# Kernel tuning notes

Hardware: AMD Instinct MI355X
Metric: run time of the kernel (lower is better)

The kernel has to match this reference:

```python
import jax, jax.numpy as jnp
import numpy as np

B, T, C, H = 4, 1024, 1024, 16
D = C // H
EPS = 1e-5


def _ln(x, g, b):
    mu = jnp.mean(x, axis=-1, keepdims=True)
    var = jnp.mean((x - mu) ** 2, axis=-1, keepdims=True)
    return (x - mu) * jax.lax.rsqrt(var + EPS) * g + b


def _attn(xq, xkv, wq, wk, wv, wo, bo, mask):
    # wq/wk/wv/wo: [C, C] (in, out). Dropout is identity in eval mode.
    Bq, Tq, _ = xq.shape
    Tk = xkv.shape[1]
    q = (xq @ wq).reshape(Bq, Tq, H, D)
    k = (xkv @ wk).reshape(Bq, Tk, H, D)
    v = (xkv @ wv).reshape(Bq, Tk, H, D)
    scores = jnp.einsum('bqhd,bkhd->bhqk', q, k) / jnp.sqrt(jnp.float32(D))
    if mask is not None:
        scores = jnp.where(mask == 0, -jnp.inf, scores)
    p = jax.nn.softmax(scores, axis=-1)
    out = jnp.einsum('bhqk,bkhd->bqhd', p, v).reshape(Bq, Tq, C)
    return out @ wo + bo


def setup_inputs() -> dict:
    key = jax.random.key(0)
    ks = jax.random.split(key, 20)
    s = 0.02
    inp = {
        'x': jax.random.normal(ks[0], (B, T, C), jnp.float32),
        'encoder_out': jax.random.normal(ks[1], (B, T, C), jnp.float32),
        'sa_wq': jax.random.normal(ks[2], (C, C), jnp.float32) * s,
        'sa_wk': jax.random.normal(ks[3], (C, C), jnp.float32) * s,
        'sa_wv': jax.random.normal(ks[4], (C, C), jnp.float32) * s,
        'sa_wo': jax.random.normal(ks[5], (C, C), jnp.float32) * s,
        'sa_bo': jnp.zeros((C,), jnp.float32),
        'ca_wq': jax.random.normal(ks[6], (C, C), jnp.float32) * s,
        'ca_wk': jax.random.normal(ks[7], (C, C), jnp.float32) * s,
        'ca_wv': jax.random.normal(ks[8], (C, C), jnp.float32) * s,
        'ca_wo': jax.random.normal(ks[9], (C, C), jnp.float32) * s,
        'ca_bo': jnp.zeros((C,), jnp.float32),
        'ff_w1': jax.random.normal(ks[10], (C, 4 * C), jnp.float32) * s,
        'ff_b1': jnp.zeros((4 * C,), jnp.float32),
        'ff_w2': jax.random.normal(ks[11], (4 * C, C), jnp.float32) * s,
        'ff_b2': jnp.zeros((C,), jnp.float32),
        'ln1_g': jnp.ones((C,), jnp.float32), 'ln1_b': jnp.zeros((C,), jnp.float32),
        'ln2_g': jnp.ones((C,), jnp.float32), 'ln2_b': jnp.zeros((C,), jnp.float32),
        'ln3_g': jnp.ones((C,), jnp.float32), 'ln3_b': jnp.zeros((C,), jnp.float32),
        'tgt_mask': jnp.tril(jnp.ones((T, T), jnp.int32))[None, None],  # [1,1,T,T] causal
        'src_mask': jnp.ones((B, 1, 1, T), jnp.int32),
    }
    return inp


def reference(x, encoder_out, sa_wq, sa_wk, sa_wv, sa_wo, sa_bo,
              ca_wq, ca_wk, ca_wv, ca_wo, ca_bo,
              ff_w1, ff_b1, ff_w2, ff_b2,
              ln1_g, ln1_b, ln2_g, ln2_b, ln3_g, ln3_b,
              tgt_mask, src_mask):
    # self-attention (masked) + residual
    x = x + _attn(_ln(x, ln1_g, ln1_b), _ln(x, ln1_g, ln1_b),
                  sa_wq, sa_wk, sa_wv, sa_wo, sa_bo, tgt_mask)
    # cross-attention + residual (only src_mask applied to scores)
    h = _ln(x, ln2_g, ln2_b)
    x = x + _attn(h, encoder_out, ca_wq, ca_wk, ca_wv, ca_wo, ca_bo, src_mask)
    # FFN + residual
    h = _ln(x, ln3_g, ln3_b)
    x = x + (jax.nn.relu(h @ ff_w1 + ff_b1) @ ff_w2 + ff_b2)
    return x
```

## Files before the change

kernel.cpp:

```cpp
#include <hip/hip_runtime.h>

typedef __bf16 bf16_t;
typedef __bf16 bf16x4 __attribute__((ext_vector_type(4)));
typedef __bf16 bf16x8 __attribute__((ext_vector_type(8)));
typedef float  f32x4  __attribute__((ext_vector_type(4)));

#define LN_EPS 1e-5f

__device__ __forceinline__ void g2l16(const bf16_t* g, bf16_t* l) {
    __builtin_amdgcn_global_load_lds(
        (const __attribute__((address_space(1))) void*)g,
        (__attribute__((address_space(3))) void*)l, 16, 0, 0);
}

__global__ __launch_bounds__(256) void cvt_kernel(
    const float* __restrict__ x, bf16_t* __restrict__ y)
{
    int i = blockIdx.x * 256 + threadIdx.x;
    f32x4 v = ((const f32x4*)x)[i];
    bf16x4 o = { (bf16_t)v.x, (bf16_t)v.y, (bf16_t)v.z, (bf16_t)v.w };
    ((bf16x4*)y)[i] = o;
}

struct WT16 {
    const float* src[16]; bf16_t* dst[16];
    int srcN[16]; int dstK[16]; int k0b[16]; int n0b[16];
};

__global__ __launch_bounds__(256) void wt16_kernel(WT16 p)
{
    const int z = blockIdx.z;
    const float* W = p.src[z];
    bf16_t* Wt = p.dst[z];
    const int N = p.srcN[z], Kd = p.dstK[z];
    const int n0 = p.n0b[z] + blockIdx.x * 64, k0 = p.k0b[z] + blockIdx.y * 64;
    __shared__ float ts[64][65];
    const int tid = threadIdx.x;
#pragma unroll
    for (int it = 0; it < 4; ++it) {
        int f = tid + it * 256;
        int row = f >> 4, c4 = (f & 15) * 4;
        f32x4 v = *(const f32x4*)(W + (size_t)(k0 + row) * N + n0 + c4);
        ts[row][c4 + 0] = v.x; ts[row][c4 + 1] = v.y;
        ts[row][c4 + 2] = v.z; ts[row][c4 + 3] = v.w;
    }
    __syncthreads();
#pragma unroll
    for (int it = 0; it < 4; ++it) {
        int f = tid + it * 256;
        int nrow = f >> 4, k4 = (f & 15) * 4;
        bf16x4 o = { (bf16_t)ts[k4 + 0][nrow], (bf16_t)ts[k4 + 1][nrow],
                     (bf16_t)ts[k4 + 2][nrow], (bf16_t)ts[k4 + 3][nrow] };
        *(bf16x4*)(Wt + (size_t)(n0 + nrow) * Kd + k0 + k4) = o;
    }
}

__global__ __launch_bounds__(256) void ln_kernel(
    const float* __restrict__ x, const float* __restrict__ g,
    const float* __restrict__ b, bf16_t* __restrict__ y)
{
    const int row = blockIdx.x;
    const int tid = threadIdx.x;
    const f32x4* xr = (const f32x4*)(x + (size_t)row * 1024);
    f32x4 v = xr[tid];
    float s  = v.x + v.y + v.z + v.w;
    float s2 = v.x*v.x + v.y*v.y + v.z*v.z + v.w*v.w;
#pragma unroll
    for (int off = 1; off < 64; off <<= 1) {
        s  += __shfl_xor(s,  off, 64);
        s2 += __shfl_xor(s2, off, 64);
    }
    __shared__ float ws_[4], ws2_[4];
    const int wave = tid >> 6, lane = tid & 63;
    if (lane == 0) { ws_[wave] = s; ws2_[wave] = s2; }
    __syncthreads();
    s  = ws_[0] + ws_[1] + ws_[2] + ws_[3];
    s2 = ws2_[0] + ws2_[1] + ws2_[2] + ws2_[3];
    const float mu   = s  * (1.0f/1024.0f);
    const float var  = s2 * (1.0f/1024.0f) - mu*mu;
    const float rstd = rsqrtf(var + LN_EPS);
    f32x4 gv = ((const f32x4*)g)[tid];
    f32x4 bv = ((const f32x4*)b)[tid];
    f32x4 o  = (v - mu) * rstd * gv + bv;
    bf16x4 ob = { (bf16_t)o.x, (bf16_t)o.y, (bf16_t)o.z, (bf16_t)o.w };
    ((bf16x4*)(y + (size_t)row * 1024))[tid] = ob;
}

template<int BN, int DEPTH, int OUT_BF16, int HAS_BIAS, int DO_RELU, int HAS_RES>
__global__ __launch_bounds__(256) void gemm_bf16(
    const bf16_t* __restrict__ A, const bf16_t* __restrict__ Bt,
    const float* __restrict__ bias, const float* __restrict__ res,
    void* __restrict__ out, int M, int N, int K)
{
    constexpr int NT = BN / 32;
    __shared__ __align__(16) bf16_t As[2][DEPTH][128 * 32];
    __shared__ __align__(16) bf16_t Bs[2][DEPTH][BN * 32];

    const int tid  = threadIdx.x;
    const int wave = tid >> 6, lane = tid & 63;
    const int q    = lane >> 4, r = lane & 15;
    const int wm   = wave >> 1, wn = wave & 1;

    const int nbx  = gridDim.x;
    const int id   = blockIdx.y * nbx + blockIdx.x;
    const int mper = gridDim.y >> 3;
    const int jj   = id >> 3;
    const int bm   = (id & 7) * mper + jj / nbx;
    const int bn   = jj % nbx;
    const int m0   = bm * 128, n0 = bn * BN;

    const int srow = lane >> 2;
    const int schk = (lane & 3) * 8;

    auto stage = [&](int buf, int kk) {
#pragma unroll
        for (int s = 0; s < DEPTH; ++s) {
#pragma unroll
            for (int t = 0; t < 2; ++t) {
                int rowA = wave * 32 + t * 16;
                g2l16(A + (size_t)(m0 + rowA + srow) * K + kk + s * 32 + schk,
                      &As[buf][s][rowA * 32]);
            }
#pragma unroll
            for (int t = 0; t < BN / 64; ++t) {
                int rowB = wave * (BN / 4) + t * 16;
                g2l16(Bt + (size_t)(n0 + rowB + srow) * K + kk + s * 32 + schk,
                      &Bs[buf][s][rowB * 32]);
            }
        }
    };

    f32x4 acc[4][NT] = {};
    constexpr int STEP = 32 * DEPTH;
    stage(0, 0);

    for (int kk = 0; kk < K; kk += STEP) {
        const int cur = (kk / STEP) & 1;
        __syncthreads();
        if (kk + STEP < K) stage(cur ^ 1, kk + STEP);
#pragma unroll
        for (int s = 0; s < DEPTH; ++s) {
            bf16x8 af[4], bf[NT];
#pragma unroll
            for (int i = 0; i < 4; ++i)
                af[i] = *(const bf16x8*)&As[cur][s][(wm * 64 + i * 16 + r) * 32 + q * 8];
#pragma unroll
            for (int j = 0; j < NT; ++j)
                bf[j] = *(const bf16x8*)&Bs[cur][s][(wn * 16 * NT + j * 16 + r) * 32 + q * 8];
#pragma unroll
            for (int i = 0; i < 4; ++i)
#pragma unroll
                for (int j = 0; j < NT; ++j)
                    acc[i][j] = __builtin_amdgcn_mfma_f32_16x16x32_bf16(af[i], bf[j], acc[i][j], 0, 0, 0);
        }
    }

#pragma unroll
    for (int i = 0; i < 4; ++i)
#pragma unroll
        for (int j = 0; j < NT; ++j)
#pragma unroll
            for (int e = 0; e < 4; ++e) {
                int row = m0 + wm * 64 + i * 16 + q * 4 + e;
                int col = n0 + wn * 16 * NT + j * 16 + r;
                float v = acc[i][j][e];
                if (HAS_BIAS) v += bias[col];
                if (DO_RELU)  v = v > 0.0f ? v : 0.0f;
                if (HAS_RES)  v += res[(size_t)row * N + col];
                if (OUT_BF16) ((bf16_t*)out)[(size_t)row * N + col] = (bf16_t)v;
                else          ((float*)out)[(size_t)row * N + col] = v;
            }
}

__global__ __launch_bounds__(256) void gemm_qkv3(
    const bf16_t* __restrict__ Aq, const bf16_t* __restrict__ Akv,
    const bf16_t* __restrict__ Wt3,
    bf16_t* __restrict__ outq, bf16_t* __restrict__ outk,
    bf16_t* __restrict__ vt)
{
    const int K = 1024;
    __shared__ __align__(16) bf16_t As[2][128 * 32];
    __shared__ __align__(16) bf16_t Bs[2][128 * 32];

    const int tid  = threadIdx.x;
    const int wave = tid >> 6, lane = tid & 63;
    const int q    = lane >> 4, r = lane & 15;
    const int wm   = wave >> 1, wn = wave & 1;

    const int nbx  = gridDim.x;
    const int id   = blockIdx.y * nbx + blockIdx.x;
    const int mper = gridDim.y >> 3;
    const int jj   = id >> 3;
    const int bm   = (id & 7) * mper + jj / nbx;
    const int bn   = jj % nbx;
    const int m0   = bm * 128, n0 = bn * 128;
    const int grp  = bn >> 3;
    const bf16_t* A = (grp == 0) ? Aq : Akv;

    const int srow = lane >> 2;
    const int schk = (lane & 3) * 8;

    auto stage = [&](int buf, int kk) {
#pragma unroll
        for (int t = 0; t < 2; ++t) {
            int row = wave * 32 + t * 16;
            g2l16(A   + (size_t)(m0 + row + srow) * K + kk + schk, &As[buf][row * 32]);
            g2l16(Wt3 + (size_t)(n0 + row + srow) * K + kk + schk, &Bs[buf][row * 32]);
        }
    };

    f32x4 acc[4][4] = {};
    stage(0, 0);

    for (int kk = 0; kk < K; kk += 32) {
        const int cur = (kk >> 5) & 1;
        __syncthreads();
        if (kk + 32 < K) stage(cur ^ 1, kk + 32);

        bf16x8 af[4], bf[4];
#pragma unroll
        for (int i = 0; i < 4; ++i)
            af[i] = *(const bf16x8*)&As[cur][(wm * 64 + i * 16 + r) * 32 + q * 8];
#pragma unroll
        for (int j = 0; j < 4; ++j)
            bf[j] = *(const bf16x8*)&Bs[cur][(wn * 64 + j * 16 + r) * 32 + q * 8];
#pragma unroll
        for (int i = 0; i < 4; ++i)
#pragma unroll
            for (int j = 0; j < 4; ++j)
                acc[i][j] = __builtin_amdgcn_mfma_f32_16x16x32_bf16(af[i], bf[j], acc[i][j], 0, 0, 0);
    }

    if (grp < 2) {
        bf16_t* o = (grp == 0) ? outq : outk;
        const float sc = (grp == 0) ? 0.125f : 1.0f;
        const int c0 = n0 - grp * 1024;
#pragma unroll
        for (int i = 0; i < 4; ++i)
#pragma unroll
            for (int j = 0; j < 4; ++j)
#pragma unroll
                for (int e = 0; e < 4; ++e) {
                    int row = m0 + wm * 64 + i * 16 + q * 4 + e;
                    int col = c0 + wn * 64 + j * 16 + r;
                    o[(size_t)row * 1024 + col] = (bf16_t)(acc[i][j][e] * sc);
                }
    } else {
#pragma unroll
        for (int i = 0; i < 4; ++i)
#pragma unroll
            for (int j = 0; j < 4; ++j) {
                int c = (n0 - 2048) + wn * 64 + j * 16 + r;
                int hh = c >> 6, d = c & 63;
                int row0 = m0 + wm * 64 + i * 16 + q * 4;
                int bb = row0 >> 10, t = row0 & 1023;
                bf16x4 pk = { (bf16_t)acc[i][j][0], (bf16_t)acc[i][j][1],
                              (bf16_t)acc[i][j][2], (bf16_t)acc[i][j][3] };
                *(bf16x4*)&vt[((size_t)((bb << 4) + hh) * 64 + d) * 1024 + t] = pk;
            }
    }
}

template<int CAUSAL>
__global__ __launch_bounds__(256) void attn_mfma_kernel(
    const bf16_t* __restrict__ Qp, const bf16_t* __restrict__ Kp,
    const bf16_t* __restrict__ VTp, bf16_t* __restrict__ Op)
{
    const int T = 1024;
    const int LP = 72;
    __shared__ __align__(16) bf16_t Ps[128 * LP];
    __shared__ __align__(16) bf16_t Ks[2][2][64 * 32];
    __shared__ __align__(16) bf16_t Vs[2][2][64 * 32];

    const int id  = blockIdx.x + 8 * (blockIdx.y + 16 * blockIdx.z);
    const int jj  = id >> 3;
    const int pr  = (id & 7) * 8 + (jj >> 3);
    const int qt  = jj & 7;
    const int h   = pr & 15, b = pr >> 4;

    const int tid  = threadIdx.x;
    const int wave = tid >> 6, lane = tid & 63;
    const int q    = lane >> 4, r = lane & 15;
    const int srow = lane >> 2, schk = (lane & 3) * 8;

    const bf16_t* Kb = Kp + (size_t)(b * T) * 1024 + h * 64;
    const bf16_t* Vb = VTp + (size_t)((b * 16 + h) * 64) * 1024;

    auto stageKV = [&](int buf, int kt) {
#pragma unroll
        for (int ks = 0; ks < 2; ++ks) {
            g2l16(Kb + (size_t)(kt * 64 + wave * 16 + srow) * 1024 + ks * 32 + schk,
                  &Ks[buf][ks][wave * 16 * 32]);
            g2l16(Vb + (size_t)(wave * 16 + srow) * 1024 + kt * 64 + ks * 32 + schk,
                  &Vs[buf][ks][wave * 16 * 32]);
        }
    };

    {
        const bf16_t* Qb = Qp + (size_t)(b * T + qt * 128) * 1024 + h * 64;
#pragma unroll
        for (int it = 0; it < 4; ++it) {
            int f = tid + it * 256;
            int row = f >> 3, c8 = (f & 7) * 8;
            *(bf16x8*)&Ps[row * LP + c8] = *(const bf16x8*)(Qb + (size_t)row * 1024 + c8);
        }
    }
    __syncthreads();
    bf16x8 qa[2][2];
#pragma unroll
    for (int mt = 0; mt < 2; ++mt)
#pragma unroll
        for (int ks = 0; ks < 2; ++ks)
            qa[mt][ks] = *(const bf16x8*)&Ps[(wave * 32 + mt * 16 + r) * LP + ks * 32 + q * 8];

    const bf16_t one_b = (bf16_t)1.0f;
    const bf16x8 ones = { one_b, one_b, one_b, one_b, one_b, one_b, one_b, one_b };

    f32x4 o[2][4] = {};
    f32x4 ol[2] = {};

    const int nk = CAUSAL ? (2 * qt + 2) : 16;
    stageKV(0, 0);

    for (int kt = 0; kt < nk; ++kt) {
        const int cur = kt & 1;
        __syncthreads();
        if (kt + 1 < nk) stageKV(cur ^ 1, kt + 1);

        f32x4 s[2][4] = {};
#pragma unroll
        for (int ks = 0; ks < 2; ++ks)
#pragma unroll
            for (int nt = 0; nt < 4; ++nt) {
                bf16x8 kb = *(const bf16x8*)&Ks[cur][ks][(nt * 16 + r) * 32 + q * 8];
#pragma unroll
                for (int mt = 0; mt < 2; ++mt)
                    s[mt][nt] = __builtin_amdgcn_mfma_f32_16x16x32_bf16(qa[mt][ks], kb, s[mt][nt], 0, 0, 0);
            }

        if (CAUSAL) {
#pragma unroll
            for (int mt = 0; mt < 2; ++mt) {
                const int r0 = qt * 128 + wave * 32 + mt * 16;
                if (kt * 64 + 63 > r0) {
#pragma unroll
                    for (int nt = 0; nt < 4; ++nt) {
                        int kg = kt * 64 + nt * 16 + r;
#pragma unroll
                        for (int i2 = 0; i2 < 4; ++i2)
                            if (kg > r0 + q * 4 + i2) s[mt][nt][i2] = -INFINITY;
                    }
                }
            }
        }

#pragma unroll
        for (int mt = 0; mt < 2; ++mt)
#pragma unroll
            for (int nt = 0; nt < 4; ++nt)
#pragma unroll
                for (int i2 = 0; i2 < 4; ++i2)
                    Ps[(wave * 32 + mt * 16 + q * 4 + i2) * LP + nt * 16 + r] =
                        (bf16_t)__expf(s[mt][nt][i2]);

#pragma unroll
        for (int ks = 0; ks < 2; ++ks) {
            bf16x8 pa[2];
#pragma unroll
            for (int mt = 0; mt < 2; ++mt)
                pa[mt] = *(const bf16x8*)&Ps[(wave * 32 + mt * 16 + r) * LP + ks * 32 + q * 8];
#pragma unroll
            for (int dt = 0; dt < 4; ++dt) {
                bf16x8 vb = *(const bf16x8*)&Vs[cur][ks][(dt * 16 + r) * 32 + q * 8];
#pragma unroll
                for (int mt = 0; mt < 2; ++mt)
                    o[mt][dt] = __builtin_amdgcn_mfma_f32_16x16x32_bf16(pa[mt], vb, o[mt][dt], 0, 0, 0);
            }
#pragma unroll
            for (int mt = 0; mt < 2; ++mt)
                ol[mt] = __builtin_amdgcn_mfma_f32_16x16x32_bf16(pa[mt], ones, ol[mt], 0, 0, 0);
        }
    }

    bf16_t* Ob = Op + (size_t)(b * T + qt * 128 + wave * 32) * 1024 + h * 64;
#pragma unroll
    for (int mt = 0; mt < 2; ++mt) {
        f32x4 inv;
#pragma unroll
        for (int i2 = 0; i2 < 4; ++i2) inv[i2] = 1.0f / ol[mt][i2];
#pragma unroll
        for (int dt = 0; dt < 4; ++dt)
#pragma unroll
            for (int i2 = 0; i2 < 4; ++i2)
                Ob[(size_t)(mt * 16 + q * 4 + i2) * 1024 + dt * 16 + r] = (bf16_t)(o[mt][dt][i2] * inv[i2]);
    }
}

extern "C" void kernel_launch(void* const* d_in, const int* in_sizes, int n_in,
                              void* d_out, int out_size, void* d_ws, size_t ws_size,
                              hipStream_t stream)
{
    const float* x     = (const float*)d_in[0];
    const float* enc   = (const float*)d_in[1];
    const float* sa_wq = (const float*)d_in[2];
    const float* sa_wk = (const float*)d_in[3];
    const float* sa_wv = (const float*)d_in[4];
    const float* sa_wo = (const float*)d_in[5];
    const float* sa_bo = (const float*)d_in[6];
    const float* ca_wq = (const float*)d_in[7];
    const float* ca_wk = (const float*)d_in[8];
    const float* ca_wv = (const float*)d_in[9];
    const float* ca_wo = (const float*)d_in[10];
    const float* ca_bo = (const float*)d_in[11];
    const float* ff_w1 = (const float*)d_in[12];
    const float* ff_b1 = (const float*)d_in[13];
    const float* ff_w2 = (const float*)d_in[14];
    const float* ff_b2 = (const float*)d_in[15];
    const float* ln1_g = (const float*)d_in[16];
    const float* ln1_b = (const float*)d_in[17];
    const float* ln2_g = (const float*)d_in[18];
    const float* ln2_b = (const float*)d_in[19];
    const float* ln3_g = (const float*)d_in[20];
    const float* ln3_b = (const float*)d_in[21];

    float* out = (float*)d_out;
    char* ws = (char*)d_ws;
    const size_t MB = 1024 * 1024;
    bf16_t* w_s3  = (bf16_t*)(ws +  0 * MB);
    bf16_t* w_so  = (bf16_t*)(ws +  6 * MB);
    bf16_t* w_c3  = (bf16_t*)(ws +  8 * MB);
    bf16_t* w_co  = (bf16_t*)(ws + 14 * MB);
    bf16_t* w_f1  = (bf16_t*)(ws + 16 * MB);
    bf16_t* w_f2  = (bf16_t*)(ws + 24 * MB);
    bf16_t* b_enc = (bf16_t*)(ws + 32 * MB);
    bf16_t* b_ln  = (bf16_t*)(ws + 40 * MB);
    bf16_t* b_q   = (bf16_t*)(ws + 48 * MB);
    bf16_t* b_k   = (bf16_t*)(ws + 56 * MB);
    bf16_t* b_vt  = (bf16_t*)(ws + 64 * MB);
    bf16_t* b_at  = (bf16_t*)(ws + 72 * MB);
    float*  b_x1  = (float*) (ws + 80 * MB);
    float*  b_x2  = (float*) (ws + 48 * MB);
    bf16_t* b_h1  = (bf16_t*)(ws + 64 * MB);

    const int M = 4096;
    dim3 blk(256);

    WT16 wp;
    const float* srcs[8] = { sa_wq, sa_wk, sa_wv, sa_wo, ca_wq, ca_wk, ca_wv, ca_wo };
    bf16_t* dsts[8] = { w_s3, w_s3 + 1024*1024, w_s3 + 2048*1024, w_so,
                        w_c3, w_c3 + 1024*1024, w_c3 + 2048*1024, w_co };
    for (int z = 0; z < 8; ++z) {
        wp.src[z] = srcs[z]; wp.dst[z] = dsts[z];
        wp.srcN[z] = 1024; wp.dstK[z] = 1024; wp.k0b[z] = 0; wp.n0b[z] = 0;
    }
    for (int z = 8; z < 12; ++z) {
        wp.src[z] = ff_w1; wp.dst[z] = w_f1;
        wp.srcN[z] = 4096; wp.dstK[z] = 1024; wp.k0b[z] = 0; wp.n0b[z] = (z - 8) * 1024;
    }
    for (int z = 12; z < 16; ++z) {
        wp.src[z] = ff_w2; wp.dst[z] = w_f2;
        wp.srcN[z] = 1024; wp.dstK[z] = 4096; wp.k0b[z] = (z - 12) * 1024; wp.n0b[z] = 0;
    }
    wt16_kernel<<<dim3(16, 16, 16), blk, 0, stream>>>(wp);
    cvt_kernel<<<4096, blk, 0, stream>>>(enc, b_enc);

    ln_kernel<<<4096, blk, 0, stream>>>(x, ln1_g, ln1_b, b_ln);
    gemm_qkv3<<<dim3(24, 32), blk, 0, stream>>>(b_ln, b_ln, w_s3, b_q, b_k, b_vt);
    attn_mfma_kernel<1><<<dim3(8, 16, 4), blk, 0, stream>>>(b_q, b_k, b_vt, b_at);
    gemm_bf16<64,2,0,1,0,1><<<dim3(16, 32), blk, 0, stream>>>(
        b_at, w_so, sa_bo, x, b_x1, M, 1024, 1024);
    ln_kernel<<<4096, blk, 0, stream>>>(b_x1, ln2_g, ln2_b, b_ln);
    gemm_qkv3<<<dim3(24, 32), blk, 0, stream>>>(b_ln, b_enc, w_c3, b_q, b_k, b_vt);
    attn_mfma_kernel<0><<<dim3(8, 16, 4), blk, 0, stream>>>(b_q, b_k, b_vt, b_at);
    gemm_bf16<64,2,0,1,0,1><<<dim3(16, 32), blk, 0, stream>>>(
        b_at, w_co, ca_bo, b_x1, b_x2, M, 1024, 1024);
    ln_kernel<<<4096, blk, 0, stream>>>(b_x2, ln3_g, ln3_b, b_ln);
    gemm_bf16<128,1,1,1,1,0><<<dim3(32, 32), blk, 0, stream>>>(
        b_ln, w_f1, ff_b1, nullptr, b_h1, M, 4096, 1024);
    gemm_bf16<64,2,0,1,0,1><<<dim3(16, 32), blk, 0, stream>>>(
        b_h1, w_f2, ff_b2, b_x2, out, M, 1024, 4096);
}
```

Before: 482.9 us.

## Deepen GEMM LDS pipelines with vmcnt waits, swizzled LDS, and MFMA priority

```diff
diff --git a/kernel.cpp b/kernel.cpp
--- a/kernel.cpp
+++ b/kernel.cpp
@@ -11,6 +11,19 @@
     __builtin_amdgcn_global_load_lds(
         (const __attribute__((address_space(1))) void*)g,
         (__attribute__((address_space(3))) void*)l, 16, 0, 0);
+}
+
+template<int N> __device__ __forceinline__ void wait_vm() {
+    if constexpr (N == 0)      asm volatile("s_waitcnt vmcnt(0)" ::: "memory");
+    else if constexpr (N == 3) asm volatile("s_waitcnt vmcnt(3)" ::: "memory");
+    else if constexpr (N == 4) asm volatile("s_waitcnt vmcnt(4)" ::: "memory");
+    else if constexpr (N == 6) asm volatile("s_waitcnt vmcnt(6)" ::: "memory");
+    else if constexpr (N == 8) asm volatile("s_waitcnt vmcnt(8)" ::: "memory");
+    else                       asm volatile("s_waitcnt vmcnt(0)" ::: "memory");
+}
+__device__ __forceinline__ void block_bar() {
+    __builtin_amdgcn_s_barrier();
+    asm volatile("" ::: "memory");
 }
 
 __global__ __launch_bounds__(256) void cvt_kernel(
@@ -86,15 +99,16 @@
     ((bf16x4*)(y + (size_t)row * 1024))[tid] = ob;
 }
 
-template<int BN, int DEPTH, int OUT_BF16, int HAS_BIAS, int DO_RELU, int HAS_RES>
+template<int BN, int NBUF, int OUT_BF16, int HAS_BIAS, int DO_RELU, int HAS_RES>
 __global__ __launch_bounds__(256) void gemm_bf16(
     const bf16_t* __restrict__ A, const bf16_t* __restrict__ Bt,
     const float* __restrict__ bias, const float* __restrict__ res,
     void* __restrict__ out, int M, int N, int K)
 {
     constexpr int NT = BN / 32;
-    __shared__ __align__(16) bf16_t As[2][DEPTH][128 * 32];
-    __shared__ __align__(16) bf16_t Bs[2][DEPTH][BN * 32];
+    constexpr int L  = 2 + BN / 64;
+    __shared__ __align__(16) bf16_t As[NBUF][128 * 32];
+    __shared__ __align__(16) bf16_t Bs[NBUF][BN * 32];
 
     const int tid  = threadIdx.x;
     const int wave = tid >> 6, lane = tid & 63;
@@ -110,49 +124,62 @@
     const int m0   = bm * 128, n0 = bn * BN;
 
     const int srow = lane >> 2;
-    const int schk = (lane & 3) * 8;
+    const int schk = ((lane & 3) ^ ((lane >> 3) & 3)) * 8;
+    const int rsw  = ((r >> 1) & 3) * 8;
 
     auto stage = [&](int buf, int kk) {
 #pragma unroll
-        for (int s = 0; s < DEPTH; ++s) {
-#pragma unroll
-            for (int t = 0; t < 2; ++t) {
-                int rowA = wave * 32 + t * 16;
-                g2l16(A + (size_t)(m0 + rowA + srow) * K + kk + s * 32 + schk,
-                      &As[buf][s][rowA * 32]);
-            }
-#pragma unroll
-            for (int t = 0; t < BN / 64; ++t) {
-                int rowB = wave * (BN / 4) + t * 16;
-                g2l16(Bt + (size_t)(n0 + rowB + srow) * K + kk + s * 32 + schk,
-                      &Bs[buf][s][rowB * 32]);
-            }
+        for (int t = 0; t < 2; ++t) {
+            int rowA = wave * 32 + t * 16;
+            g2l16(A + (size_t)(m0 + rowA + srow) * K + kk + schk,
+                  &As[buf][rowA * 32]);
+        }
+#pragma unroll
+        for (int t = 0; t < BN / 64; ++t) {
+            int rowB = wave * (BN / 4) + t * 16;
+            g2l16(Bt + (size_t)(n0 + rowB + srow) * K + kk + schk,
+                  &Bs[buf][rowB * 32]);
         }
     };
 
     f32x4 acc[4][NT] = {};
-    constexpr int STEP = 32 * DEPTH;
-    stage(0, 0);
-
-    for (int kk = 0; kk < K; kk += STEP) {
-        const int cur = (kk / STEP) & 1;
-        __syncthreads();
-        if (kk + STEP < K) stage(cur ^ 1, kk + STEP);
-#pragma unroll
-        for (int s = 0; s < DEPTH; ++s) {
-            bf16x8 af[4], bf[NT];
-#pragma unroll
-            for (int i = 0; i < 4; ++i)
-                af[i] = *(const bf16x8*)&As[cur][s][(wm * 64 + i * 16 + r) * 32 + q * 8];
+
+    auto compute = [&](int b) {
+        bf16x8 af[4], bfr[NT];
+#pragma unroll
+        for (int i = 0; i < 4; ++i)
+            af[i] = *(const bf16x8*)&As[b][(wm * 64 + i * 16 + r) * 32 + (q * 8 ^ rsw)];
+#pragma unroll
+        for (int j = 0; j < NT; ++j)
+            bfr[j] = *(const bf16x8*)&Bs[b][(wn * 16 * NT + j * 16 + r) * 32 + (q * 8 ^ rsw)];
+        __builtin_amdgcn_s_setprio(1);
+#pragma unroll
+        for (int i = 0; i < 4; ++i)
 #pragma unroll
             for (int j = 0; j < NT; ++j)
-                bf[j] = *(const bf16x8*)&Bs[cur][s][(wn * 16 * NT + j * 16 + r) * 32 + q * 8];
-#pragma unroll
-            for (int i = 0; i < 4; ++i)
-#pragma unroll
-                for (int j = 0; j < NT; ++j)
-                    acc[i][j] = __builtin_amdgcn_mfma_f32_16x16x32_bf16(af[i], bf[j], acc[i][j], 0, 0, 0);
-        }
+                acc[i][j] = __builtin_amdgcn_mfma_f32_16x16x32_bf16(af[i], bfr[j], acc[i][j], 0, 0, 0);
+        __builtin_amdgcn_s_setprio(0);
+    };
+
+    int ks = 0;
+#pragma unroll
+    for (int p = 0; p < NBUF - 1; ++p) { stage(p, ks); ks += 32; }
+
+    const int NK = K >> 5;
+    int cur = 0, sb = NBUF - 1;
+    for (int t = 0; t < NK - (NBUF - 2); ++t) {
+        wait_vm<L * (NBUF - 2)>();
+        block_bar();
+        if (ks < K) { stage(sb, ks); ks += 32; sb = (sb + 1 == NBUF) ? 0 : sb + 1; }
+        compute(cur);
+        cur = (cur + 1 == NBUF) ? 0 : cur + 1;
+    }
+#pragma unroll
+    for (int e = NBUF - 3; e >= 0; --e) {
+        if (e >= 1) wait_vm<L>(); else wait_vm<0>();
+        block_bar();
+        compute(cur);
+        cur = (cur + 1 == NBUF) ? 0 : cur + 1;
     }
 
 #pragma unroll
@@ -179,8 +206,10 @@
     bf16_t* __restrict__ vt)
 {
     const int K = 1024;
-    __shared__ __align__(16) bf16_t As[2][128 * 32];
-    __shared__ __align__(16) bf16_t Bs[2][128 * 32];
+    constexpr int NBUF = 3;
+    constexpr int L = 4;
+    __shared__ __align__(16) bf16_t As[NBUF][128 * 32];
+    __shared__ __align__(16) bf16_t Bs[NBUF][128 * 32];
 
     const int tid  = threadIdx.x;
     const int wave = tid >> 6, lane = tid & 63;
@@ -198,7 +227,8 @@
     const bf16_t* A = (grp == 0) ? Aq : Akv;
 
     const int srow = lane >> 2;
-    const int schk = (lane & 3) * 8;
+    const int schk = ((lane & 3) ^ ((lane >> 3) & 3)) * 8;
+    const int rsw  = ((r >> 1) & 3) * 8;
 
     auto stage = [&](int buf, int kk) {
 #pragma unroll
@@ -210,26 +240,40 @@
     };
 
     f32x4 acc[4][4] = {};
-    stage(0, 0);
-
-    for (int kk = 0; kk < K; kk += 32) {
-        const int cur = (kk >> 5) & 1;
-        __syncthreads();
-        if (kk + 32 < K) stage(cur ^ 1, kk + 32);
-
-        bf16x8 af[4], bf[4];
+
+    auto compute = [&](int b) {
+        bf16x8 af[4], bfr[4];
 #pragma unroll
         for (int i = 0; i < 4; ++i)
-            af[i] = *(const bf16x8*)&As[cur][(wm * 64 + i * 16 + r) * 32 + q * 8];
+            af[i] = *(const bf16x8*)&As[b][(wm * 64 + i * 16 + r) * 32 + (q * 8 ^ rsw)];
 #pragma unroll
         for (int j = 0; j < 4; ++j)
-            bf[j] = *(const bf16x8*)&Bs[cur][(wn * 64 + j * 16 + r) * 32 + q * 8];
+            bfr[j] = *(const bf16x8*)&Bs[b][(wn * 64 + j * 16 + r) * 32 + (q * 8 ^ rsw)];
+        __builtin_amdgcn_s_setprio(1);
 #pragma unroll
         for (int i = 0; i < 4; ++i)
 #pragma unroll
             for (int j = 0; j < 4; ++j)
-                acc[i][j] = __builtin_amdgcn_mfma_f32_16x16x32_bf16(af[i], bf[j], acc[i][j], 0, 0, 0);
-    }
+                acc[i][j] = __builtin_amdgcn_mfma_f32_16x16x32_bf16(af[i], bfr[j], acc[i][j], 0, 0, 0);
+        __builtin_amdgcn_s_setprio(0);
+    };
+
+    int ks = 0;
+#pragma unroll
+    for (int p = 0; p < NBUF - 1; ++p) { stage(p, ks); ks += 32; }
+
+    const int NK = K >> 5;
+    int cur = 0, sb = NBUF - 1;
+    for (int t = 0; t < NK - (NBUF - 2); ++t) {
+        wait_vm<L * (NBUF - 2)>();
+        block_bar();
+        if (ks < K) { stage(sb, ks); ks += 32; sb = (sb + 1 == NBUF) ? 0 : sb + 1; }
+        compute(cur);
+        cur = (cur + 1 == NBUF) ? 0 : cur + 1;
+    }
+    wait_vm<0>();
+    block_bar();
+    compute(cur);
 
     if (grp < 2) {
         bf16_t* o = (grp == 0) ? outq : outk;
@@ -467,16 +511,16 @@
     ln_kernel<<<4096, blk, 0, stream>>>(x, ln1_g, ln1_b, b_ln);
     gemm_qkv3<<<dim3(24, 32), blk, 0, stream>>>(b_ln, b_ln, w_s3, b_q, b_k, b_vt);
     attn_mfma_kernel<1><<<dim3(8, 16, 4), blk, 0, stream>>>(b_q, b_k, b_vt, b_at);
-    gemm_bf16<64,2,0,1,0,1><<<dim3(16, 32), blk, 0, stream>>>(
+    gemm_bf16<64,4,0,1,0,1><<<dim3(16, 32), blk, 0, stream>>>(
         b_at, w_so, sa_bo, x, b_x1, M, 1024, 1024);
     ln_kernel<<<4096, blk, 0, stream>>>(b_x1, ln2_g, ln2_b, b_ln);
     gemm_qkv3<<<dim3(24, 32), blk, 0, stream>>>(b_ln, b_enc, w_c3, b_q, b_k, b_vt);
     attn_mfma_kernel<0><<<dim3(8, 16, 4), blk, 0, stream>>>(b_q, b_k, b_vt, b_at);
-    gemm_bf16<64,2,0,1,0,1><<<dim3(16, 32), blk, 0, stream>>>(
+    gemm_bf16<64,4,0,1,0,1><<<dim3(16, 32), blk, 0, stream>>>(
         b_at, w_co, ca_bo, b_x1, b_x2, M, 1024, 1024);
     ln_kernel<<<4096, blk, 0, stream>>>(b_x2, ln3_g, ln3_b, b_ln);
-    gemm_bf16<128,1,1,1,1,0><<<dim3(32, 32), blk, 0, stream>>>(
+    gemm_bf16<128,3,1,1,1,0><<<dim3(32, 32), blk, 0, stream>>>(
         b_ln, w_f1, ff_b1, nullptr, b_h1, M, 4096, 1024);
-    gemm_bf16<64,2,0,1,0,1><<<dim3(16, 32), blk, 0, stream>>>(
+    gemm_bf16<64,4,0,1,0,1><<<dim3(16, 32), blk, 0, stream>>>(
         b_h1, w_f2, ff_b2, b_x2, out, M, 1024, 4096);
 }
```

Measured after the change: 493.9 us. 1.02x slower.

## Swizzle LDS tiles in GEMMs and split-K the FFN down-projection with atomics

Applied to the files above, without the earlier changes.

```diff
diff --git a/kernel.cpp b/kernel.cpp
--- a/kernel.cpp
+++ b/kernel.cpp
@@ -20,6 +20,12 @@
     f32x4 v = ((const f32x4*)x)[i];
     bf16x4 o = { (bf16_t)v.x, (bf16_t)v.y, (bf16_t)v.z, (bf16_t)v.w };
     ((bf16x4*)y)[i] = o;
+}
+
+__global__ __launch_bounds__(256) void zero_kernel(float* __restrict__ p)
+{
+    f32x4 z = { 0.f, 0.f, 0.f, 0.f };
+    ((f32x4*)p)[blockIdx.x * 256 + threadIdx.x] = z;
 }
 
 struct WT16 {
@@ -86,7 +92,8 @@
     ((bf16x4*)(y + (size_t)row * 1024))[tid] = ob;
 }
 
-template<int BN, int DEPTH, int OUT_BF16, int HAS_BIAS, int DO_RELU, int HAS_RES>
+template<int BN, int DEPTH, int OUT_BF16, int HAS_BIAS, int DO_RELU, int HAS_RES,
+         int SPLITK>
 __global__ __launch_bounds__(256) void gemm_bf16(
     const bf16_t* __restrict__ A, const bf16_t* __restrict__ Bt,
     const float* __restrict__ bias, const float* __restrict__ res,
@@ -110,7 +117,8 @@
     const int m0   = bm * 128, n0 = bn * BN;
 
     const int srow = lane >> 2;
-    const int schk = (lane & 3) * 8;
+    const int schk = ((lane & 3) ^ ((lane >> 3) & 3)) * 8;
+    const int rsw  = ((r >> 1) & 3) * 8;
 
     auto stage = [&](int buf, int kk) {
 #pragma unroll
@@ -132,26 +140,28 @@
 
     f32x4 acc[4][NT] = {};
     constexpr int STEP = 32 * DEPTH;
-    stage(0, 0);
-
-    for (int kk = 0; kk < K; kk += STEP) {
+    const int Kc    = K / SPLITK;
+    const int kbase = (SPLITK > 1) ? blockIdx.z * Kc : 0;
+    stage(0, kbase);
+
+    for (int kk = 0; kk < Kc; kk += STEP) {
         const int cur = (kk / STEP) & 1;
         __syncthreads();
-        if (kk + STEP < K) stage(cur ^ 1, kk + STEP);
+        if (kk + STEP < Kc) stage(cur ^ 1, kbase + kk + STEP);
 #pragma unroll
         for (int s = 0; s < DEPTH; ++s) {
-            bf16x8 af[4], bf[NT];
+            bf16x8 af[4], bfr[NT];
 #pragma unroll
             for (int i = 0; i < 4; ++i)
-                af[i] = *(const bf16x8*)&As[cur][s][(wm * 64 + i * 16 + r) * 32 + q * 8];
+                af[i] = *(const bf16x8*)&As[cur][s][(wm * 64 + i * 16 + r) * 32 + (q * 8 ^ rsw)];
 #pragma unroll
             for (int j = 0; j < NT; ++j)
-                bf[j] = *(const bf16x8*)&Bs[cur][s][(wn * 16 * NT + j * 16 + r) * 32 + q * 8];
+                bfr[j] = *(const bf16x8*)&Bs[cur][s][(wn * 16 * NT + j * 16 + r) * 32 + (q * 8 ^ rsw)];
 #pragma unroll
             for (int i = 0; i < 4; ++i)
 #pragma unroll
                 for (int j = 0; j < NT; ++j)
-                    acc[i][j] = __builtin_amdgcn_mfma_f32_16x16x32_bf16(af[i], bf[j], acc[i][j], 0, 0, 0);
+                    acc[i][j] = __builtin_amdgcn_mfma_f32_16x16x32_bf16(af[i], bfr[j], acc[i][j], 0, 0, 0);
         }
     }
 
@@ -164,11 +174,19 @@
                 int row = m0 + wm * 64 + i * 16 + q * 4 + e;
                 int col = n0 + wn * 16 * NT + j * 16 + r;
                 float v = acc[i][j][e];
-                if (HAS_BIAS) v += bias[col];
-                if (DO_RELU)  v = v > 0.0f ? v : 0.0f;
-                if (HAS_RES)  v += res[(size_t)row * N + col];
-                if (OUT_BF16) ((bf16_t*)out)[(size_t)row * N + col] = (bf16_t)v;
-                else          ((float*)out)[(size_t)row * N + col] = v;
+                if (SPLITK == 1) {
+                    if (HAS_BIAS) v += bias[col];
+                    if (DO_RELU)  v = v > 0.0f ? v : 0.0f;
+                    if (HAS_RES)  v += res[(size_t)row * N + col];
+                    if (OUT_BF16) ((bf16_t*)out)[(size_t)row * N + col] = (bf16_t)v;
+                    else          ((float*)out)[(size_t)row * N + col] = v;
+                } else {
+                    if (blockIdx.z == 0) {
+                        if (HAS_BIAS) v += bias[col];
+                        if (HAS_RES)  v += res[(size_t)row * N + col];
+                    }
+                    atomicAdd(&((float*)out)[(size_t)row * N + col], v);
+                }
             }
 }
 
@@ -198,7 +216,8 @@
     const bf16_t* A = (grp == 0) ? Aq : Akv;
 
     const int srow = lane >> 2;
-    const int schk = (lane & 3) * 8;
+    const int schk = ((lane & 3) ^ ((lane >> 3) & 3)) * 8;
+    const int rsw  = ((r >> 1) & 3) * 8;
 
     auto stage = [&](int buf, int kk) {
 #pragma unroll
@@ -217,18 +236,18 @@
         __syncthreads();
         if (kk + 32 < K) stage(cur ^ 1, kk + 32);
 
-        bf16x8 af[4], bf[4];
+        bf16x8 af[4], bfr[4];
 #pragma unroll
         for (int i = 0; i < 4; ++i)
-            af[i] = *(const bf16x8*)&As[cur][(wm * 64 + i * 16 + r) * 32 + q * 8];
+            af[i] = *(const bf16x8*)&As[cur][(wm * 64 + i * 16 + r) * 32 + (q * 8 ^ rsw)];
 #pragma unroll
         for (int j = 0; j < 4; ++j)
-            bf[j] = *(const bf16x8*)&Bs[cur][(wn * 64 + j * 16 + r) * 32 + q * 8];
+            bfr[j] = *(const bf16x8*)&Bs[cur][(wn * 64 + j * 16 + r) * 32 + (q * 8 ^ rsw)];
 #pragma unroll
         for (int i = 0; i < 4; ++i)
 #pragma unroll
             for (int j = 0; j < 4; ++j)
-                acc[i][j] = __builtin_amdgcn_mfma_f32_16x16x32_bf16(af[i], bf[j], acc[i][j], 0, 0, 0);
+                acc[i][j] = __builtin_amdgcn_mfma_f32_16x16x32_bf16(af[i], bfr[j], acc[i][j], 0, 0, 0);
     }
 
     if (grp < 2) {
@@ -445,6 +464,8 @@
     const int M = 4096;
     dim3 blk(256);
 
+    zero_kernel<<<4096, blk, 0, stream>>>(out);
+
     WT16 wp;
     const float* srcs[8] = { sa_wq, sa_wk, sa_wv, sa_wo, ca_wq, ca_wk, ca_wv, ca_wo };
     bf16_t* dsts[8] = { w_s3, w_s3 + 1024*1024, w_s3 + 2048*1024, w_so,
@@ -467,16 +488,16 @@
     ln_kernel<<<4096, blk, 0, stream>>>(x, ln1_g, ln1_b, b_ln);
     gemm_qkv3<<<dim3(24, 32), blk, 0, stream>>>(b_ln, b_ln, w_s3, b_q, b_k, b_vt);
     attn_mfma_kernel<1><<<dim3(8, 16, 4), blk, 0, stream>>>(b_q, b_k, b_vt, b_at);
-    gemm_bf16<64,2,0,1,0,1><<<dim3(16, 32), blk, 0, stream>>>(
+    gemm_bf16<64,2,0,1,0,1,1><<<dim3(16, 32), blk, 0, stream>>>(
         b_at, w_so, sa_bo, x, b_x1, M, 1024, 1024);
     ln_kernel<<<4096, blk, 0, stream>>>(b_x1, ln2_g, ln2_b, b_ln);
     gemm_qkv3<<<dim3(24, 32), blk, 0, stream>>>(b_ln, b_enc, w_c3, b_q, b_k, b_vt);
     attn_mfma_kernel<0><<<dim3(8, 16, 4), blk, 0, stream>>>(b_q, b_k, b_vt, b_at);
-    gemm_bf16<64,2,0,1,0,1><<<dim3(16, 32), blk, 0, stream>>>(
+    gemm_bf16<64,2,0,1,0,1,1><<<dim3(16, 32), blk, 0, stream>>>(
         b_at, w_co, ca_bo, b_x1, b_x2, M, 1024, 1024);
     ln_kernel<<<4096, blk, 0, stream>>>(b_x2, ln3_g, ln3_b, b_ln);
-    gemm_bf16<128,1,1,1,1,0><<<dim3(32, 32), blk, 0, stream>>>(
+    gemm_bf16<128,1,1,1,1,0,1><<<dim3(32, 32), blk, 0, stream>>>(
         b_ln, w_f1, ff_b1, nullptr, b_h1, M, 4096, 1024);
-    gemm_bf16<64,2,0,1,0,1><<<dim3(16, 32), blk, 0, stream>>>(
+    gemm_bf16<128,1,0,1,0,1,4><<<dim3(8, 32, 4), blk, 0, stream>>>(
         b_h1, w_f2, ff_b2, b_x2, out, M, 1024, 4096);
 }
```

Measured after the change: 513.9 us. 1.06x slower.
